# Kernel optimization log

Measured on AMD Instinct MI355X. Metric: run time of the kernel, lower is better.

The kernel has to match this reference:

```python
import jax, jax.numpy as jnp
import numpy as np

GROUP = 128  # quantization group size along the input dimension


def dequant(q, scales, zeros):
    # q: [out, in] int4 codes stored as int32 in [0,16)
    # scales, zeros: [out, in//GROUP] per-group affine params
    out_dim, in_dim = q.shape
    g = in_dim // GROUP
    w = (q.astype(jnp.float32).reshape(out_dim, g, GROUP) - zeros[:, :, None]) * scales[:, :, None]
    return w.reshape(out_dim, in_dim)


def setup_inputs() -> dict:
    key = jax.random.key(0)
    ks = jax.random.split(key, 10)
    H, I = 4096, 11008
    B, S = 64, 1
    inp = {
        "x": jax.random.normal(ks[0], (B, S, H), dtype=jnp.float32),
        "gate_qweight": jax.random.randint(ks[1], (I, H), 0, 16, dtype=jnp.int32),
        "gate_scales": jax.random.uniform(ks[2], (I, H // GROUP), dtype=jnp.float32) * 0.02,
        "gate_zeros": jax.random.uniform(ks[3], (I, H // GROUP), dtype=jnp.float32) * 16.0,
        "up_qweight": jax.random.randint(ks[4], (I, H), 0, 16, dtype=jnp.int32),
        "up_scales": jax.random.uniform(ks[5], (I, H // GROUP), dtype=jnp.float32) * 0.02,
        "up_zeros": jax.random.uniform(ks[6], (I, H // GROUP), dtype=jnp.float32) * 16.0,
        "down_qweight": jax.random.randint(ks[7], (H, I), 0, 16, dtype=jnp.int32),
        "down_scales": jax.random.uniform(ks[8], (H, I // GROUP), dtype=jnp.float32) * 0.02,
        "down_zeros": jax.random.uniform(ks[9], (H, I // GROUP), dtype=jnp.float32) * 16.0,
    }
    return inp


def reference(x, gate_qweight, gate_scales, gate_zeros,
              up_qweight, up_scales, up_zeros,
              down_qweight, down_scales, down_zeros):
    Wg = dequant(gate_qweight, gate_scales, gate_zeros)   # [I, H]
    Wu = dequant(up_qweight, up_scales, up_zeros)         # [I, H]
    Wd = dequant(down_qweight, down_scales, down_zeros)   # [H, I]
    gate = jnp.einsum('bsh,ih->bsi', x, Wg)
    up = jnp.einsum('bsh,ih->bsi', x, Wu)
    h = jax.nn.silu(gate) * up                             # SwiGLU
    return jnp.einsum('bsi,hi->bsh', h, Wd)
```

## Files before the change

kernel.cpp:

```cpp
#include <hip/hip_runtime.h>
#include <hip/hip_bf16.h>
#include <stdint.h>

#define H_DIM 4096
#define I_DIM 11008
#define NGH   32
#define NGI   86
#define HP    (H_DIM/8)
#define IP    (I_DIM/8)

typedef __attribute__((ext_vector_type(8))) short short8;
typedef __attribute__((ext_vector_type(4))) short s16x4;
typedef __attribute__((ext_vector_type(4))) float f32x4;
typedef __attribute__((ext_vector_type(4))) int   i32x4;

static __device__ __forceinline__ short f2bf(float f) {
  union { __hip_bfloat16 b; short s; } u;
  u.b = __float2bfloat16(f);
  return u.s;
}

__global__ void xcvt_kernel(const float* __restrict__ x, short* __restrict__ xb) {
  int i = (blockIdx.x * 256 + threadIdx.x) * 4;
  f32x4 v = *(const f32x4*)(x + i);
  s16x4 o;
  o[0] = f2bf(v[0]); o[1] = f2bf(v[1]); o[2] = f2bf(v[2]); o[3] = f2bf(v[3]);
  *(s16x4*)(xb + i) = o;
}

__global__ __launch_bounds__(256) void pack_kernel(const int* __restrict__ src,
                                                   int* __restrict__ dst) {
  const int o = blockIdx.x * 256 + threadIdx.x;
  const int* s = src + (size_t)o * 8;
  i32x4 a = *(const i32x4*)s;
  i32x4 b = *(const i32x4*)(s + 4);
  int p = (a[0] & 15)        | ((a[1] & 15) << 4)  | ((a[2] & 15) << 8)  | ((a[3] & 15) << 12)
        | ((b[0] & 15) << 16) | ((b[1] & 15) << 20) | ((b[2] & 15) << 24) | ((b[3] & 15) << 28);
  dst[o] = p;
}

__global__ __launch_bounds__(512, 4) void phase1p_kernel(
    const short* __restrict__ xb,
    const int* __restrict__ gp, const float* __restrict__ gsc, const float* __restrict__ gze,
    const int* __restrict__ up, const float* __restrict__ usc, const float* __restrict__ uze,
    short* __restrict__ hb)
{
  __shared__ float red[8][4][4][64];
  const int n0   = blockIdx.x * 16;
  const int w    = threadIdx.x >> 6;
  const int l    = threadIdx.x & 63;
  const int col  = l & 15;
  const int krow = l >> 4;
  const int i    = n0 + col;

  const int*   gpr = gp + (size_t)i * HP;
  const int*   upr = up + (size_t)i * HP;
  const float* gsr = gsc + (size_t)i * NGH;
  const float* gzr = gze + (size_t)i * NGH;
  const float* usr = usc + (size_t)i * NGH;
  const float* uzr = uze + (size_t)i * NGH;

  f32x4 accG[4], accU[4];
#pragma unroll
  for (int c = 0; c < 4; ++c)
#pragma unroll
    for (int r = 0; r < 4; ++r) { accG[c][r] = 0.f; accU[c][r] = 0.f; }

  const int wb = w * 64;

  int qg = gpr[wb + krow];
  int qu = upr[wb + krow];

#pragma unroll 1
  for (int g = 0; g < 4; ++g) {
    const int gg = w * 4 + g;
    const float sg = gsr[gg], zg = gzr[gg] * sg;
    const float su = usr[gg], zu = uzr[gg] * su;
#pragma unroll
    for (int ks = 0; ks < 4; ++ks) {
      const int cg = qg, cu = qu;
      const int wloc = g * 16 + ks * 4;
      {
        const int nw = wb + ((wloc + 4) & 63) + krow;
        qg = gpr[nw];
        qu = upr[nw];
      }
      const int kg = w * 512 + g * 128 + ks * 32 + krow * 8;
      short8 a[4];
#pragma unroll
      for (int c = 0; c < 4; ++c)
        a[c] = *(const short8*)(xb + (size_t)(c * 16 + col) * H_DIM + kg);
      short8 bg, bu;
#pragma unroll
      for (int j = 0; j < 8; ++j) {
        bg[j] = f2bf((float)((cg >> (4 * j)) & 15) * sg - zg);
        bu[j] = f2bf((float)((cu >> (4 * j)) & 15) * su - zu);
      }
#pragma unroll
      for (int c = 0; c < 4; ++c) {
        accG[c] = __builtin_amdgcn_mfma_f32_16x16x32_bf16(a[c], bg, accG[c], 0, 0, 0);
        accU[c] = __builtin_amdgcn_mfma_f32_16x16x32_bf16(a[c], bu, accU[c], 0, 0, 0);
      }
    }
  }

  const int c2 = threadIdx.x >> 7;
  const int rh = (threadIdx.x >> 6) & 1;
  const int ll = threadIdx.x & 63;

#pragma unroll
  for (int c = 0; c < 4; ++c)
#pragma unroll
    for (int r = 0; r < 4; ++r)
      red[w][c][r][l] = accG[c][r];
  __syncthreads();
  float gsum[2];
#pragma unroll
  for (int rr = 0; rr < 2; ++rr) {
    const int r = rh * 2 + rr;
    float s = 0.f;
#pragma unroll
    for (int ww = 0; ww < 8; ++ww) s += red[ww][c2][r][ll];
    gsum[rr] = s;
  }
  __syncthreads();

#pragma unroll
  for (int c = 0; c < 4; ++c)
#pragma unroll
    for (int r = 0; r < 4; ++r)
      red[w][c][r][l] = accU[c][r];
  __syncthreads();
#pragma unroll
  for (int rr = 0; rr < 2; ++rr) {
    const int r = rh * 2 + rr;
    float us = 0.f;
#pragma unroll
    for (int ww = 0; ww < 8; ++ww) us += red[ww][c2][r][ll];
    const float gv = gsum[rr];
    const float hv = gv / (1.f + __expf(-gv)) * us;
    const int m  = c2 * 16 + (ll >> 4) * 4 + r;
    const int ii = n0 + (ll & 15);
    hb[(size_t)m * I_DIM + ii] = f2bf(hv);
  }
}

__global__ __launch_bounds__(512, 4) void phase2p_kernel(
    const short* __restrict__ hb,
    const int* __restrict__ dp, const float* __restrict__ dsc, const float* __restrict__ dze,
    float* __restrict__ part)
{
  __shared__ float red[8][4][4][64];
  const int tile  = blockIdx.x & 255;
  const int split = blockIdx.x >> 8;
  const int n0   = tile * 16;
  const int w    = threadIdx.x >> 6;
  const int l    = threadIdx.x & 63;
  const int col  = l & 15;
  const int krow = l >> 4;
  const int n    = n0 + col;

  const int*   dpr = dp + (size_t)n * IP;
  const float* dsr = dsc + (size_t)n * NGI;
  const float* dzr = dze + (size_t)n * NGI;

  f32x4 acc[4];
#pragma unroll
  for (int c = 0; c < 4; ++c)
#pragma unroll
    for (int r = 0; r < 4; ++r) acc[c][r] = 0.f;

  const int cnt    = (w < 6) ? 11 : 10;
  const int sstart = (w < 6) ? w * 11 : 66 + (w - 6) * 10;
  const int kbase  = split * 2752 + sstart * 32;
  const int wbase  = split * 344 + sstart * 4;

  int gprev = -1;
  float sv = 0.f, zv = 0.f;

  int qd = dpr[wbase + krow];
#pragma unroll 1
  for (int s = 0; s < cnt; ++s) {
    const int cd = qd;
    {
      const int ns = (s + 1 < cnt) ? (s + 1) : 0;
      qd = dpr[wbase + ns * 4 + krow];
    }
    const int k0 = kbase + s * 32;
    const int g  = k0 >> 7;
    if (g != gprev) { sv = dsr[g]; zv = dzr[g] * sv; gprev = g; }
    short8 a[4];
#pragma unroll
    for (int c = 0; c < 4; ++c)
      a[c] = *(const short8*)(hb + (size_t)(c * 16 + col) * I_DIM + k0 + krow * 8);
    short8 b;
#pragma unroll
    for (int j = 0; j < 8; ++j)
      b[j] = f2bf((float)((cd >> (4 * j)) & 15) * sv - zv);
#pragma unroll
    for (int c = 0; c < 4; ++c)
      acc[c] = __builtin_amdgcn_mfma_f32_16x16x32_bf16(a[c], b, acc[c], 0, 0, 0);
  }

#pragma unroll
  for (int c = 0; c < 4; ++c)
#pragma unroll
    for (int r = 0; r < 4; ++r)
      red[w][c][r][l] = acc[c][r];
  __syncthreads();

  if (threadIdx.x < 256) {
    const int c2 = threadIdx.x >> 6;
    const int ll = threadIdx.x & 63;
    float* po = part + (size_t)split * (64 * H_DIM);
#pragma unroll
    for (int r = 0; r < 4; ++r) {
      float s = 0.f;
#pragma unroll
      for (int ww = 0; ww < 8; ++ww) s += red[ww][c2][r][ll];
      const int m  = c2 * 16 + (ll >> 4) * 4 + r;
      const int nn = n0 + (ll & 15);
      po[(size_t)m * H_DIM + nn] = s;
    }
  }
}

__global__ void reduce4_kernel(const float* __restrict__ part, float* __restrict__ out) {
  const int idx = (blockIdx.x * 256 + threadIdx.x) * 4;
  const int S = 64 * H_DIM;
  f32x4 s0 = *(const f32x4*)(part + idx);
  f32x4 s1 = *(const f32x4*)(part + S + idx);
  f32x4 s2 = *(const f32x4*)(part + 2 * S + idx);
  f32x4 s3 = *(const f32x4*)(part + 3 * S + idx);
  f32x4 r = (s0 + s1) + (s2 + s3);
  *(f32x4*)(out + idx) = r;
}

__global__ __launch_bounds__(512, 4) void phase1f_kernel(
    const short* __restrict__ xb,
    const int* __restrict__ gq, const float* __restrict__ gsc, const float* __restrict__ gze,
    const int* __restrict__ uq, const float* __restrict__ usc, const float* __restrict__ uze,
    short* __restrict__ hb)
{
  __shared__ float red[8][4][4][64];
  const int n0   = blockIdx.x * 16;
  const int w    = threadIdx.x >> 6;
  const int l    = threadIdx.x & 63;
  const int col  = l & 15;
  const int krow = l >> 4;
  const int i    = n0 + col;
  const int*   gqr = gq + (size_t)i * H_DIM;
  const int*   uqr = uq + (size_t)i * H_DIM;
  const float* gsr = gsc + (size_t)i * NGH;
  const float* gzr = gze + (size_t)i * NGH;
  const float* usr = usc + (size_t)i * NGH;
  const float* uzr = uze + (size_t)i * NGH;
  f32x4 accG[4], accU[4];
#pragma unroll
  for (int c = 0; c < 4; ++c)
#pragma unroll
    for (int r = 0; r < 4; ++r) { accG[c][r] = 0.f; accU[c][r] = 0.f; }
  const int kw = w * 512;
  int pk = kw + krow * 8;
  i32x4 nq0 = *(const i32x4*)(gqr + pk);
  i32x4 nq1 = *(const i32x4*)(gqr + pk + 4);
  i32x4 np0 = *(const i32x4*)(uqr + pk);
  i32x4 np1 = *(const i32x4*)(uqr + pk + 4);
#pragma unroll 1
  for (int g = 0; g < 4; ++g) {
    const int gg = w * 4 + g;
    const float sg = gsr[gg], zg = gzr[gg] * sg;
    const float su = usr[gg], zu = uzr[gg] * su;
#pragma unroll
    for (int ks = 0; ks < 4; ++ks) {
      i32x4 q0 = nq0, q1 = nq1, p0 = np0, p1 = np1;
      const int klocal = g * 128 + ks * 32;
      {
        const int nk = kw + ((klocal + 32) & 511) + krow * 8;
        nq0 = *(const i32x4*)(gqr + nk);
        nq1 = *(const i32x4*)(gqr + nk + 4);
        np0 = *(const i32x4*)(uqr + nk);
        np1 = *(const i32x4*)(uqr + nk + 4);
      }
      const int koff = kw + klocal + krow * 8;
      short8 a[4];
#pragma unroll
      for (int c = 0; c < 4; ++c)
        a[c] = *(const short8*)(xb + (size_t)(c * 16 + col) * H_DIM + koff);
      short8 bg, bu;
#pragma unroll
      for (int j = 0; j < 4; ++j) {
        bg[j]     = f2bf((float)q0[j] * sg - zg);
        bg[j + 4] = f2bf((float)q1[j] * sg - zg);
        bu[j]     = f2bf((float)p0[j] * su - zu);
        bu[j + 4] = f2bf((float)p1[j] * su - zu);
      }
#pragma unroll
      for (int c = 0; c < 4; ++c) {
        accG[c] = __builtin_amdgcn_mfma_f32_16x16x32_bf16(a[c], bg, accG[c], 0, 0, 0);
        accU[c] = __builtin_amdgcn_mfma_f32_16x16x32_bf16(a[c], bu, accU[c], 0, 0, 0);
      }
    }
  }
  const int c2 = threadIdx.x >> 7;
  const int rh = (threadIdx.x >> 6) & 1;
  const int ll = threadIdx.x & 63;
#pragma unroll
  for (int c = 0; c < 4; ++c)
#pragma unroll
    for (int r = 0; r < 4; ++r)
      red[w][c][r][l] = accG[c][r];
  __syncthreads();
  float gsum[2];
#pragma unroll
  for (int rr = 0; rr < 2; ++rr) {
    const int r = rh * 2 + rr;
    float s = 0.f;
#pragma unroll
    for (int ww = 0; ww < 8; ++ww) s += red[ww][c2][r][ll];
    gsum[rr] = s;
  }
  __syncthreads();
#pragma unroll
  for (int c = 0; c < 4; ++c)
#pragma unroll
    for (int r = 0; r < 4; ++r)
      red[w][c][r][l] = accU[c][r];
  __syncthreads();
#pragma unroll
  for (int rr = 0; rr < 2; ++rr) {
    const int r = rh * 2 + rr;
    float us = 0.f;
#pragma unroll
    for (int ww = 0; ww < 8; ++ww) us += red[ww][c2][r][ll];
    const float gv = gsum[rr];
    const float hv = gv / (1.f + __expf(-gv)) * us;
    const int m  = c2 * 16 + (ll >> 4) * 4 + r;
    const int ii = n0 + (ll & 15);
    hb[(size_t)m * I_DIM + ii] = f2bf(hv);
  }
}

__global__ __launch_bounds__(512, 4) void phase2f_kernel(
    const short* __restrict__ hb,
    const int* __restrict__ dq, const float* __restrict__ dsc, const float* __restrict__ dze,
    float* __restrict__ part)
{
  __shared__ float red[8][4][4][64];
  const int tile  = blockIdx.x & 255;
  const int split = blockIdx.x >> 8;
  const int n0   = tile * 16;
  const int w    = threadIdx.x >> 6;
  const int l    = threadIdx.x & 63;
  const int col  = l & 15;
  const int krow = l >> 4;
  const int n    = n0 + col;
  const int*   dqr = dq + (size_t)n * I_DIM;
  const float* dsr = dsc + (size_t)n * NGI;
  const float* dzr = dze + (size_t)n * NGI;
  f32x4 acc[4];
#pragma unroll
  for (int c = 0; c < 4; ++c)
#pragma unroll
    for (int r = 0; r < 4; ++r) acc[c][r] = 0.f;
  const int cnt    = (w < 6) ? 11 : 10;
  const int sstart = (w < 6) ? w * 11 : 66 + (w - 6) * 10;
  const int kbase  = split * 2752 + sstart * 32;
  int gprev = -1;
  float sv = 0.f, zv = 0.f;
  int pk = kbase + krow * 8;
  i32x4 nq0 = *(const i32x4*)(dqr + pk);
  i32x4 nq1 = *(const i32x4*)(dqr + pk + 4);
#pragma unroll 1
  for (int s = 0; s < cnt; ++s) {
    i32x4 q0 = nq0, q1 = nq1;
    {
      const int ns = (s + 1 < cnt) ? (s + 1) : 0;
      const int nk = kbase + ns * 32 + krow * 8;
      nq0 = *(const i32x4*)(dqr + nk);
      nq1 = *(const i32x4*)(dqr + nk + 4);
    }
    const int k0 = kbase + s * 32;
    const int g  = k0 >> 7;
    if (g != gprev) { sv = dsr[g]; zv = dzr[g] * sv; gprev = g; }
    short8 a[4];
#pragma unroll
    for (int c = 0; c < 4; ++c)
      a[c] = *(const short8*)(hb + (size_t)(c * 16 + col) * I_DIM + k0 + krow * 8);
    short8 b;
#pragma unroll
    for (int j = 0; j < 4; ++j) {
      b[j]     = f2bf((float)q0[j] * sv - zv);
      b[j + 4] = f2bf((float)q1[j] * sv - zv);
    }
#pragma unroll
    for (int c = 0; c < 4; ++c)
      acc[c] = __builtin_amdgcn_mfma_f32_16x16x32_bf16(a[c], b, acc[c], 0, 0, 0);
  }
#pragma unroll
  for (int c = 0; c < 4; ++c)
#pragma unroll
    for (int r = 0; r < 4; ++r)
      red[w][c][r][l] = acc[c][r];
  __syncthreads();
  if (threadIdx.x < 256) {
    const int c2 = threadIdx.x >> 6;
    const int ll = threadIdx.x & 63;
    float* po = part + (size_t)split * (64 * H_DIM);
#pragma unroll
    for (int r = 0; r < 4; ++r) {
      float s = 0.f;
#pragma unroll
      for (int ww = 0; ww < 8; ++ww) s += red[ww][c2][r][ll];
      const int m  = c2 * 16 + (ll >> 4) * 4 + r;
      const int nn = n0 + (ll & 15);
      po[(size_t)m * H_DIM + nn] = s;
    }
  }
}

extern "C" void kernel_launch(void* const* d_in, const int* in_sizes, int n_in,
                              void* d_out, int out_size, void* d_ws, size_t ws_size,
                              hipStream_t stream) {
  const float* x  = (const float*)d_in[0];
  const int*   gq = (const int*)d_in[1];
  const float* gs = (const float*)d_in[2];
  const float* gz = (const float*)d_in[3];
  const int*   uq = (const int*)d_in[4];
  const float* us = (const float*)d_in[5];
  const float* uz = (const float*)d_in[6];
  const int*   dq = (const int*)d_in[7];
  const float* ds = (const float*)d_in[8];
  const float* dz = (const float*)d_in[9];
  float* out = (float*)d_out;

  const size_t XB   = (size_t)64 * H_DIM * 2;
  const size_t HB   = (size_t)64 * I_DIM * 2;
  const size_t PART = (size_t)4 * 64 * H_DIM * 4;
  const size_t NW   = (size_t)I_DIM * HP;
  const size_t PK   = NW * 4;

  short* xb   = (short*)d_ws;
  short* hb   = (short*)((char*)d_ws + XB);
  float* part = (float*)((char*)d_ws + XB + HB);
  int*   gp   = (int*)((char*)d_ws + XB + HB + PART);
  int*   upk  = (int*)((char*)d_ws + XB + HB + PART + PK);
  int*   dpk  = (int*)((char*)d_ws + XB + HB + PART + 2 * PK);

  xcvt_kernel<<<(64 * H_DIM) / 1024, 256, 0, stream>>>(x, xb);

  if (ws_size >= XB + HB + PART + 3 * PK) {
    const int pblk = (int)(NW / 256);
    pack_kernel<<<pblk, 256, 0, stream>>>(gq, gp);
    pack_kernel<<<pblk, 256, 0, stream>>>(uq, upk);
    phase1p_kernel<<<I_DIM / 16, 512, 0, stream>>>(xb, gp, gs, gz, upk, us, uz, hb);
    pack_kernel<<<pblk, 256, 0, stream>>>(dq, dpk);
    phase2p_kernel<<<(H_DIM / 16) * 4, 512, 0, stream>>>(hb, dpk, ds, dz, part);
  } else {
    phase1f_kernel<<<I_DIM / 16, 512, 0, stream>>>(xb, gq, gs, gz, uq, us, uz, hb);
    phase2f_kernel<<<(H_DIM / 16) * 4, 512, 0, stream>>>(hb, dq, ds, dz, part);
  }
  reduce4_kernel<<<(64 * H_DIM) / 1024, 256, 0, stream>>>(part, out);
}
```

Baseline: 246.6 us.

## Merge weight packing into one launch and double-buffer activations in both GEMV phases

The three int4 packing kernels become one launch that picks its source matrix per block, which removes two launches. Phase 1 now loads all per-group scales and zeros up front and fully unrolls the K loop with A/B double-buffering of both the packed weights and the bf16 activation fragments. Phase 2 does the same double-buffering, preloads up to four group scale/zero pairs and selects among them, which replaces the conditional reload inside the loop. This raises register pressure and can hurt occupancy, while the packing step still dominates memory traffic.

```diff
diff --git a/kernel.cpp b/kernel.cpp
--- a/kernel.cpp
+++ b/kernel.cpp
@@ -8,6 +8,7 @@
 #define NGI   86
 #define HP    (H_DIM/8)
 #define IP    (I_DIM/8)
+#define NWV   5636096
 
 typedef __attribute__((ext_vector_type(8))) short short8;
 typedef __attribute__((ext_vector_type(4))) short s16x4;
@@ -28,15 +29,18 @@
   *(s16x4*)(xb + i) = o;
 }
 
-__global__ __launch_bounds__(256) void pack_kernel(const int* __restrict__ src,
-                                                   int* __restrict__ dst) {
-  const int o = blockIdx.x * 256 + threadIdx.x;
-  const int* s = src + (size_t)o * 8;
+__global__ __launch_bounds__(256) void pack3_kernel(
+    const int* __restrict__ gq, const int* __restrict__ uq, const int* __restrict__ dq,
+    int* __restrict__ dst) {
+  const int m = blockIdx.x / 22016;
+  const int* src = (m == 0) ? gq : (m == 1) ? uq : dq;
+  const size_t o = (size_t)(blockIdx.x - m * 22016) * 256 + threadIdx.x;
+  const int* s = src + o * 8;
   i32x4 a = *(const i32x4*)s;
   i32x4 b = *(const i32x4*)(s + 4);
-  int p = (a[0] & 15)        | ((a[1] & 15) << 4)  | ((a[2] & 15) << 8)  | ((a[3] & 15) << 12)
+  int p = (a[0] & 15)         | ((a[1] & 15) << 4)  | ((a[2] & 15) << 8)  | ((a[3] & 15) << 12)
         | ((b[0] & 15) << 16) | ((b[1] & 15) << 20) | ((b[2] & 15) << 24) | ((b[3] & 15) << 28);
-  dst[o] = p;
+  dst[(size_t)m * NWV + o] = p;
 }
 
 __global__ __launch_bounds__(512, 4) void phase1p_kernel(
@@ -55,51 +59,72 @@
 
   const int*   gpr = gp + (size_t)i * HP;
   const int*   upr = up + (size_t)i * HP;
-  const float* gsr = gsc + (size_t)i * NGH;
-  const float* gzr = gze + (size_t)i * NGH;
-  const float* usr = usc + (size_t)i * NGH;
-  const float* uzr = uze + (size_t)i * NGH;
-
-  f32x4 accG[4], accU[4];
-#pragma unroll
-  for (int c = 0; c < 4; ++c)
-#pragma unroll
-    for (int r = 0; r < 4; ++r) { accG[c][r] = 0.f; accU[c][r] = 0.f; }
-
-  const int wb = w * 64;
-
-  int qg = gpr[wb + krow];
-  int qu = upr[wb + krow];
-
-#pragma unroll 1
+
+  float sgv[4], zgv[4], suv[4], zuv[4];
+#pragma unroll
   for (int g = 0; g < 4; ++g) {
     const int gg = w * 4 + g;
-    const float sg = gsr[gg], zg = gzr[gg] * sg;
-    const float su = usr[gg], zu = uzr[gg] * su;
-#pragma unroll
-    for (int ks = 0; ks < 4; ++ks) {
-      const int cg = qg, cu = qu;
-      const int wloc = g * 16 + ks * 4;
-      {
-        const int nw = wb + ((wloc + 4) & 63) + krow;
-        qg = gpr[nw];
-        qu = upr[nw];
-      }
-      const int kg = w * 512 + g * 128 + ks * 32 + krow * 8;
-      short8 a[4];
-#pragma unroll
-      for (int c = 0; c < 4; ++c)
-        a[c] = *(const short8*)(xb + (size_t)(c * 16 + col) * H_DIM + kg);
+    sgv[g] = gsc[(size_t)i * NGH + gg];
+    zgv[g] = gze[(size_t)i * NGH + gg] * sgv[g];
+    suv[g] = usc[(size_t)i * NGH + gg];
+    zuv[g] = uze[(size_t)i * NGH + gg] * suv[g];
+  }
+
+  f32x4 accG[4], accU[4];
+#pragma unroll
+  for (int c = 0; c < 4; ++c)
+#pragma unroll
+    for (int r = 0; r < 4; ++r) { accG[c][r] = 0.f; accU[c][r] = 0.f; }
+
+  const int wb = w * 64;
+  const int ks0 = w * 512 + krow * 8;
+
+  int qgA = gpr[wb + krow], quA = upr[wb + krow];
+  int qgB, quB;
+  short8 aA[4], aB[4];
+#pragma unroll
+  for (int c = 0; c < 4; ++c)
+    aA[c] = *(const short8*)(xb + (size_t)(c * 16 + col) * H_DIM + ks0);
+
+#pragma unroll
+  for (int u = 0; u < 8; ++u) {
+    const int t1 = 2 * u + 1;
+    const int t2 = (2 * u + 2) & 15;
+    const int g  = u >> 1;
+    qgB = gpr[wb + 4 * t1 + krow];
+    quB = upr[wb + 4 * t1 + krow];
+#pragma unroll
+    for (int c = 0; c < 4; ++c)
+      aB[c] = *(const short8*)(xb + (size_t)(c * 16 + col) * H_DIM + ks0 + t1 * 32);
+    {
       short8 bg, bu;
 #pragma unroll
       for (int j = 0; j < 8; ++j) {
-        bg[j] = f2bf((float)((cg >> (4 * j)) & 15) * sg - zg);
-        bu[j] = f2bf((float)((cu >> (4 * j)) & 15) * su - zu);
+        bg[j] = f2bf((float)((qgA >> (4 * j)) & 15) * sgv[g] - zgv[g]);
+        bu[j] = f2bf((float)((quA >> (4 * j)) & 15) * suv[g] - zuv[g]);
       }
 #pragma unroll
       for (int c = 0; c < 4; ++c) {
-        accG[c] = __builtin_amdgcn_mfma_f32_16x16x32_bf16(a[c], bg, accG[c], 0, 0, 0);
-        accU[c] = __builtin_amdgcn_mfma_f32_16x16x32_bf16(a[c], bu, accU[c], 0, 0, 0);
+        accG[c] = __builtin_amdgcn_mfma_f32_16x16x32_bf16(aA[c], bg, accG[c], 0, 0, 0);
+        accU[c] = __builtin_amdgcn_mfma_f32_16x16x32_bf16(aA[c], bu, accU[c], 0, 0, 0);
+      }
+    }
+    qgA = gpr[wb + 4 * t2 + krow];
+    quA = upr[wb + 4 * t2 + krow];
+#pragma unroll
+    for (int c = 0; c < 4; ++c)
+      aA[c] = *(const short8*)(xb + (size_t)(c * 16 + col) * H_DIM + ks0 + t2 * 32);
+    {
+      short8 bg, bu;
+#pragma unroll
+      for (int j = 0; j < 8; ++j) {
+        bg[j] = f2bf((float)((qgB >> (4 * j)) & 15) * sgv[g] - zgv[g]);
+        bu[j] = f2bf((float)((quB >> (4 * j)) & 15) * suv[g] - zuv[g]);
+      }
+#pragma unroll
+      for (int c = 0; c < 4; ++c) {
+        accG[c] = __builtin_amdgcn_mfma_f32_16x16x32_bf16(aB[c], bg, accG[c], 0, 0, 0);
+        accU[c] = __builtin_amdgcn_mfma_f32_16x16x32_bf16(aB[c], bu, accU[c], 0, 0, 0);
       }
     }
   }
@@ -160,9 +185,7 @@
   const int krow = l >> 4;
   const int n    = n0 + col;
 
-  const int*   dpr = dp + (size_t)n * IP;
-  const float* dsr = dsc + (size_t)n * NGI;
-  const float* dzr = dze + (size_t)n * NGI;
+  const int* dpr = dp + (size_t)n * IP;
 
   f32x4 acc[4];
 #pragma unroll
@@ -175,31 +198,72 @@
   const int kbase  = split * 2752 + sstart * 32;
   const int wbase  = split * 344 + sstart * 4;
 
-  int gprev = -1;
-  float sv = 0.f, zv = 0.f;
-
-  int qd = dpr[wbase + krow];
+  const int g0 = kbase >> 7;
+  float s0 = dsc[(size_t)n * NGI + g0];
+  float s1 = dsc[(size_t)n * NGI + min(g0 + 1, NGI - 1)];
+  float s2 = dsc[(size_t)n * NGI + min(g0 + 2, NGI - 1)];
+  float s3 = dsc[(size_t)n * NGI + min(g0 + 3, NGI - 1)];
+  float z0 = dze[(size_t)n * NGI + g0] * s0;
+  float z1 = dze[(size_t)n * NGI + min(g0 + 1, NGI - 1)] * s1;
+  float z2 = dze[(size_t)n * NGI + min(g0 + 2, NGI - 1)] * s2;
+  float z3 = dze[(size_t)n * NGI + min(g0 + 3, NGI - 1)] * s3;
+
+  int qdA = dpr[wbase + krow], qdB;
+  short8 aA[4], aB[4];
+#pragma unroll
+  for (int c = 0; c < 4; ++c)
+    aA[c] = *(const short8*)(hb + (size_t)(c * 16 + col) * I_DIM + kbase + krow * 8);
+
+  const int nh = cnt >> 1;
 #pragma unroll 1
-  for (int s = 0; s < cnt; ++s) {
-    const int cd = qd;
+  for (int u = 0; u < nh; ++u) {
+    const int t0 = 2 * u, t1 = 2 * u + 1;
+    const int t2 = (t1 + 1 < cnt) ? (t1 + 1) : 0;
+    qdB = dpr[wbase + 4 * t1 + krow];
+#pragma unroll
+    for (int c = 0; c < 4; ++c)
+      aB[c] = *(const short8*)(hb + (size_t)(c * 16 + col) * I_DIM + kbase + t1 * 32 + krow * 8);
     {
-      const int ns = (s + 1 < cnt) ? (s + 1) : 0;
-      qd = dpr[wbase + ns * 4 + krow];
-    }
-    const int k0 = kbase + s * 32;
-    const int g  = k0 >> 7;
-    if (g != gprev) { sv = dsr[g]; zv = dzr[g] * sv; gprev = g; }
-    short8 a[4];
-#pragma unroll
-    for (int c = 0; c < 4; ++c)
-      a[c] = *(const short8*)(hb + (size_t)(c * 16 + col) * I_DIM + k0 + krow * 8);
+      const int gi = ((kbase + t0 * 32) >> 7) - g0;
+      const float sv = gi == 0 ? s0 : gi == 1 ? s1 : gi == 2 ? s2 : s3;
+      const float zv = gi == 0 ? z0 : gi == 1 ? z1 : gi == 2 ? z2 : z3;
+      short8 b;
+#pragma unroll
+      for (int j = 0; j < 8; ++j)
+        b[j] = f2bf((float)((qdA >> (4 * j)) & 15) * sv - zv);
+#pragma unroll
+      for (int c = 0; c < 4; ++c)
+        acc[c] = __builtin_amdgcn_mfma_f32_16x16x32_bf16(aA[c], b, acc[c], 0, 0, 0);
+    }
+    qdA = dpr[wbase + 4 * t2 + krow];
+#pragma unroll
+    for (int c = 0; c < 4; ++c)
+      aA[c] = *(const short8*)(hb + (size_t)(c * 16 + col) * I_DIM + kbase + t2 * 32 + krow * 8);
+    {
+      const int gi = ((kbase + t1 * 32) >> 7) - g0;
+      const float sv = gi == 0 ? s0 : gi == 1 ? s1 : gi == 2 ? s2 : s3;
+      const float zv = gi == 0 ? z0 : gi == 1 ? z1 : gi == 2 ? z2 : z3;
+      short8 b;
+#pragma unroll
+      for (int j = 0; j < 8; ++j)
+        b[j] = f2bf((float)((qdB >> (4 * j)) & 15) * sv - zv);
+#pragma unroll
+      for (int c = 0; c < 4; ++c)
+        acc[c] = __builtin_amdgcn_mfma_f32_16x16x32_bf16(aB[c], b, acc[c], 0, 0, 0);
+    }
+  }
+  if (cnt & 1) {
+    const int t0 = cnt - 1;
+    const int gi = ((kbase + t0 * 32) >> 7) - g0;
+    const float sv = gi == 0 ? s0 : gi == 1 ? s1 : gi == 2 ? s2 : s3;
+    const float zv = gi == 0 ? z0 : gi == 1 ? z1 : gi == 2 ? z2 : z3;
     short8 b;
 #pragma unroll
     for (int j = 0; j < 8; ++j)
-      b[j] = f2bf((float)((cd >> (4 * j)) & 15) * sv - zv);
-#pragma unroll
-    for (int c = 0; c < 4; ++c)
-      acc[c] = __builtin_amdgcn_mfma_f32_16x16x32_bf16(a[c], b, acc[c], 0, 0, 0);
+      b[j] = f2bf((float)((qdA >> (4 * j)) & 15) * sv - zv);
+#pragma unroll
+    for (int c = 0; c < 4; ++c)
+      acc[c] = __builtin_amdgcn_mfma_f32_16x16x32_bf16(aA[c], b, acc[c], 0, 0, 0);
   }
 
 #pragma unroll
@@ -437,24 +501,21 @@
   const size_t XB   = (size_t)64 * H_DIM * 2;
   const size_t HB   = (size_t)64 * I_DIM * 2;
   const size_t PART = (size_t)4 * 64 * H_DIM * 4;
-  const size_t NW   = (size_t)I_DIM * HP;
-  const size_t PK   = NW * 4;
+  const size_t PK   = (size_t)NWV * 4;
 
   short* xb   = (short*)d_ws;
   short* hb   = (short*)((char*)d_ws + XB);
   float* part = (float*)((char*)d_ws + XB + HB);
-  int*   gp   = (int*)((char*)d_ws + XB + HB + PART);
-  int*   upk  = (int*)((char*)d_ws + XB + HB + PART + PK);
-  int*   dpk  = (int*)((char*)d_ws + XB + HB + PART + 2 * PK);
+  int*   pk   = (int*)((char*)d_ws + XB + HB + PART);
+  int*   gp   = pk;
+  int*   upk  = pk + NWV;
+  int*   dpk  = pk + 2 * (size_t)NWV;
 
   xcvt_kernel<<<(64 * H_DIM) / 1024, 256, 0, stream>>>(x, xb);
 
   if (ws_size >= XB + HB + PART + 3 * PK) {
-    const int pblk = (int)(NW / 256);
-    pack_kernel<<<pblk, 256, 0, stream>>>(gq, gp);
-    pack_kernel<<<pblk, 256, 0, stream>>>(uq, upk);
+    pack3_kernel<<<3 * 22016, 256, 0, stream>>>(gq, uq, dq, pk);
     phase1p_kernel<<<I_DIM / 16, 512, 0, stream>>>(xb, gp, gs, gz, upk, us, uz, hb);
-    pack_kernel<<<pblk, 256, 0, stream>>>(dq, dpk);
     phase2p_kernel<<<(H_DIM / 16) * 4, 512, 0, stream>>>(hb, dpk, ds, dz, part);
   } else {
     phase1f_kernel<<<I_DIM / 16, 512, 0, stream>>>(xb, gq, gs, gz, uq, us, uz, hb);
```

Result: no change. 243.0 us (-1.5%).
